# Performance work log

Measured on AMD Instinct MI355X. Metric: run time of the kernel, lower is better.

Reference implementation:

```python
import jax, jax.numpy as jnp
import numpy as np

L, M, K, H, F, D = 8, 32768, 8, 128, 32, 3  # fronts, nodes/front, in-degree, hidden, feat, depth-branches


def _resnet(x, w1, b1, w2, b2, w3, b3):
    # resnet module: lay3(tanh(lay2(tanh(lay1(x)))) + x)
    h1 = jnp.tanh(x @ w1 + b1)
    h2 = jnp.tanh(h1 @ w2 + b2)
    return (h2 + x) @ w3 + b3


def setup_inputs() -> dict:
    key = jax.random.key(0)
    ks = iter(jax.random.split(key, 80))

    def nrm(shape, fan_in):
        return jax.random.normal(next(ks), shape, jnp.float32) / np.float32(np.sqrt(fan_in))

    def bias(shape):
        return 0.01 * jax.random.normal(next(ks), shape, jnp.float32)

    inp = {}
    inp["node_feats"] = jax.random.normal(next(ks), (L, M, F), jnp.float32)
    inp["pred_idx"] = jax.random.randint(next(ks), (L - 1, M, K), 0, M, jnp.int32)
    inp["embed_w"] = nrm((F, H), F); inp["embed_b"] = bias((H,))
    # d{1,2,3}_mp_bwd and d{1,2,3}_mp_bwd1 : per-depth pair of H-resnets, stacked [D,2,...]
    inp["mp_w1"] = nrm((D, 2, H, H), H); inp["mp_b1"] = bias((D, 2, H))
    inp["mp_w2"] = nrm((D, 2, H, H), H); inp["mp_b2"] = bias((D, 2, H))
    inp["mp_w3"] = nrm((D, 2, H, H), H); inp["mp_b3"] = bias((D, 2, H))
    for p in ("comb", "node"):  # d*_comb_embed(+1), d*_node_embeds(+1)
        inp[p + "_wide_w1"] = nrm((D, 2 * H, 2 * H), 2 * H); inp[p + "_wide_b1"] = bias((D, 2 * H))
        inp[p + "_wide_w2"] = nrm((D, 2 * H, 2 * H), 2 * H); inp[p + "_wide_b2"] = bias((D, 2 * H))
        inp[p + "_wide_w3"] = nrm((D, 2 * H, H), 2 * H);     inp[p + "_wide_b3"] = bias((D, H))
        inp[p + "_h_w1"] = nrm((D, H, H), H); inp[p + "_h_b1"] = bias((D, H))
        inp[p + "_h_w2"] = nrm((D, H, H), H); inp[p + "_h_b2"] = bias((D, H))
        inp[p + "_h_w3"] = nrm((D, H, H), H); inp[p + "_h_b3"] = bias((D, H))
    return inp


def reference(node_feats, pred_idx, embed_w, embed_b,
              mp_w1, mp_b1, mp_w2, mp_b2, mp_w3, mp_b3,
              comb_wide_w1, comb_wide_b1, comb_wide_w2, comb_wide_b2, comb_wide_w3, comb_wide_b3,
              comb_h_w1, comb_h_b1, comb_h_w2, comb_h_b2, comb_h_w3, comb_h_b3,
              node_wide_w1, node_wide_b1, node_wide_w2, node_wide_b2, node_wide_w3, node_wide_b3,
              node_h_w1, node_h_b1, node_h_w2, node_h_b2, node_h_w3, node_h_b3):
    # front 0 (topological roots): apply_func only -> tanh(embed_op(feats))
    e = jnp.tanh(node_feats[0] @ embed_w + embed_b)          # [M, H]
    outs = [e]
    prev = e
    for l in range(1, L):
        d = min(l - 1, 2)                                    # bwd_depth branch (d1/d2/d3)
        # msg_func + redux_func: gather mailbox from predecessor front, sum-reduce, MLP
        s = prev[pred_idx[l - 1]].sum(axis=1)                # [M, K, H] -> [M, H]
        r = jnp.tanh(_resnet(s, mp_w1[d, 0], mp_b1[d, 0], mp_w2[d, 0], mp_b2[d, 0], mp_w3[d, 0], mp_b3[d, 0]))
        r = jnp.tanh(_resnet(r, mp_w1[d, 1], mp_b1[d, 1], mp_w2[d, 1], mp_b2[d, 1], mp_w3[d, 1], mp_b3[d, 1]))
        # apply_func: embed, comb branch (bwd_node_embeds is all-zero for not-yet-processed nodes),
        # then node_embeds branch on cat(embeds, msgs_redux)
        e = jnp.tanh(node_feats[l] @ embed_w + embed_b)
        c = jnp.concatenate([e, jnp.zeros_like(e)], axis=-1)  # [M, 2H]
        e = jnp.tanh(_resnet(c, comb_wide_w1[d], comb_wide_b1[d], comb_wide_w2[d], comb_wide_b2[d], comb_wide_w3[d], comb_wide_b3[d]))
        e = jnp.tanh(_resnet(e, comb_h_w1[d], comb_h_b1[d], comb_h_w2[d], comb_h_b2[d], comb_h_w3[d], comb_h_b3[d]))
        c2 = jnp.concatenate([e, r], axis=-1)                 # [M, 2H]
        e = jnp.tanh(_resnet(c2, node_wide_w1[d], node_wide_b1[d], node_wide_w2[d], node_wide_b2[d], node_wide_w3[d], node_wide_b3[d]))
        e = jnp.tanh(_resnet(e, node_h_w1[d], node_h_b1[d], node_h_w2[d], node_h_b2[d], node_h_w3[d], node_h_b3[d]))
        outs.append(e)
        prev = e
    return jnp.stack(outs)                                    # graph.ndata['bwd_node_embeds'] : [L, M, H]
```

## Files before the change

kernel.cpp:

```cpp
#include <hip/hip_runtime.h>
#include <hip/hip_bf16.h>

#define M_NODES 32768

using f16x8 = __attribute__((ext_vector_type(8))) _Float16;
using f16x4 = __attribute__((ext_vector_type(4))) _Float16;
using f32x4 = __attribute__((ext_vector_type(4))) float;
typedef unsigned short u16;
typedef unsigned int   u32;

__device__ __forceinline__ float h2f(u16 h){
  return (float)__builtin_bit_cast(_Float16, h);
}
__device__ __forceinline__ float tanh_fast(float x){
  float t = __builtin_amdgcn_exp2f(x * 2.8853900817779268f);
  return 1.0f - 2.0f * __builtin_amdgcn_rcpf(t + 1.0f);
}
__device__ __forceinline__ u16 f2h(float f){
  _Float16 h = (_Float16)f;
  return __builtin_bit_cast(u16, h);
}

struct PrepPtrs { const float* p[16]; };

__global__ void prep_kernel(PrepPtrs pp, u16* ws){
  const int Bc[16] = {1,6,6,6,3,3,3,3,3,3,3,3,3,3,3,3};
  const int Kc[16] = {32,128,128,128,256,256,256,128,128,128,256,256,256,128,128,128};
  const int Nc[16] = {128,128,128,128,256,256,128,128,128,128,256,256,128,128,128,128};
  const int tot = 1576960;
  for (int i = blockIdx.x*blockDim.x + threadIdx.x; i < tot; i += gridDim.x*blockDim.x){
    int e = i, s = 0;
    while (true){ int sz = Bc[s]*Kc[s]*Nc[s]; if (e < sz) break; e -= sz; ++s; }
    int K = Kc[s], N = Nc[s];
    int kn = K*N;
    int b = e / kn; int r2 = e - b*kn;
    int n = r2 / K; int k = r2 - n*K;
    float v = pp.p[s][(size_t)b*kn + (size_t)k*N + n];
    ws[i] = f2h(v);
  }
}

__global__ __launch_bounds__(256) void front0_kernel(const float* __restrict__ feats,
                                                     const float* __restrict__ ew,
                                                     const float* __restrict__ eb,
                                                     float* __restrict__ out){
  __shared__ float fl[2048];
  const int brow = blockIdx.x * 64;
  const float* f0 = feats + (size_t)brow*32;
#pragma unroll
  for (int it = 0; it < 2; ++it){
    int idx = threadIdx.x + it*256;
    *(float4*)(&fl[idx*4]) = *(const float4*)(f0 + idx*4);
  }
  __syncthreads();
  const int col = threadIdx.x & 127, rh = threadIdx.x >> 7;
  float w[32];
#pragma unroll
  for (int k = 0; k < 32; ++k) w[k] = ew[k*128 + col];
  const float bv = eb[col];
  for (int r = 0; r < 32; ++r){
    int row = rh*32 + r;
    float acc = bv;
#pragma unroll
    for (int k = 0; k < 32; ++k) acc += fl[row*32 + k] * w[k];
    out[(size_t)(brow + row)*128 + col] = tanh_fast(acc);
  }
}

struct WRing {
  const u16* wrow[4];
  f16x8 b0[4], b1[4];
};

template<int N, int WS, int NP>
__device__ __forceinline__ void wpreload(WRing& R, const u16* __restrict__ wt, int phase){
  const int tid  = threadIdx.x;
  const int lane = tid & 63, nq = tid >> 6;
  const int q = lane >> 4, c = lane & 15;
  constexpr int NT = N / 64;
  const int msk = NP - 1;
  const int p0 = phase & msk, p1 = (phase + 1) & msk;
#pragma unroll
  for (int j = 0; j < NT; ++j){
    int nt = nq*2 + (j & 1) + (j >> 1) * 8;
    R.wrow[j] = wt + (size_t)(nt*16 + c)*WS + q*8;
  }
#pragma unroll
  for (int j = 0; j < NT; ++j) R.b0[j] = *(const f16x8*)(R.wrow[j] + p0*32);
#pragma unroll
  for (int j = 0; j < NT; ++j) R.b1[j] = *(const f16x8*)(R.wrow[j] + p1*32);
}

template<int KLOOP, int N, int WS, int AMODE, int RESMODE, int OUTMODE, bool INPLACE,
         int NN, int NWS, int NNP>
__device__ __forceinline__ void mm_stage(const u16* inA, u16* outB, const u16* resB,
                                         const float* __restrict__ bias, float* gout,
                                         int phase, WRing& cur, WRing& nxt,
                                         const u16* __restrict__ wtnext)
{
  const int tid  = threadIdx.x;
  const int lane = tid & 63, nq = tid >> 6;
  const int q = lane >> 4, c = lane & 15;
  constexpr int NT = N / 64;
  constexpr int NP = KLOOP / 32;
  constexpr bool ABURST = (AMODE == 0 && NP == 4);
  const float* inAf = (const float*)inA;
  float*       outF = (float*)outB;
  const float* resF = (const float*)resB;
  const int msk = NP - 1;
  const int ph = phase & msk;

  f32x4 acc[4][NT];
#pragma unroll
  for (int m = 0; m < 4; ++m)
#pragma unroll
    for (int j = 0; j < NT; ++j) acc[m][j] = (f32x4){0.f,0.f,0.f,0.f};

  f16x8 aall[ABURST ? 16 : 1];
  if (ABURST){
#pragma unroll
    for (int kp = 0; kp < 4; ++kp){
      int kpp = (ph + kp) & 3;
#pragma unroll
      for (int m = 0; m < 4; ++m)
        aall[kp*4 + m] = *(const f16x8*)(&inA[(m*16 + c)*264 + kpp*32 + q*8]);
    }
  }

#pragma unroll
  for (int kp = 0; kp < NP; ++kp){
    const int kpp = (ph + kp) & msk;
    f16x8 bc[NT];
    if ((kp & 1) == 0){
#pragma unroll
      for (int j = 0; j < NT; ++j) bc[j] = cur.b0[j];
    } else {
#pragma unroll
      for (int j = 0; j < NT; ++j) bc[j] = cur.b1[j];
    }
    if (kp + 2 < NP){
      int kn = (ph + kp + 2) & msk;
      if ((kp & 1) == 0){
#pragma unroll
        for (int j = 0; j < NT; ++j) cur.b0[j] = *(const f16x8*)(cur.wrow[j] + kn*32);
      } else {
#pragma unroll
        for (int j = 0; j < NT; ++j) cur.b1[j] = *(const f16x8*)(cur.wrow[j] + kn*32);
      }
    }
#pragma unroll
    for (int m = 0; m < 4; ++m){
      if (AMODE == 0){
        f16x8 af;
        if (ABURST) af = aall[kp*4 + m];
        else        af = *(const f16x8*)(&inA[(m*16 + c)*264 + kpp*32 + q*8]);
#pragma unroll
        for (int j = 0; j < NT; ++j)
          acc[m][j] = __builtin_amdgcn_mfma_f32_16x16x32_f16(bc[j], af, acc[m][j], 0, 0, 0);
      } else {
        const float* ap = inAf + (m*16 + c)*132 + kpp*32 + q*8;
        float4 x0 = *(const float4*)(ap);
        float4 x1 = *(const float4*)(ap + 4);
        float xs[8] = {x0.x,x0.y,x0.z,x0.w,x1.x,x1.y,x1.z,x1.w};
        f16x8 ah, al;
#pragma unroll
        for (int k = 0; k < 8; ++k){
          _Float16 hi = (_Float16)xs[k];
          ah[k] = hi;
          al[k] = (_Float16)(xs[k] - (float)hi);
        }
#pragma unroll
        for (int j = 0; j < NT; ++j){
          acc[m][j] = __builtin_amdgcn_mfma_f32_16x16x32_f16(bc[j], ah, acc[m][j], 0, 0, 0);
          acc[m][j] = __builtin_amdgcn_mfma_f32_16x16x32_f16(bc[j], al, acc[m][j], 0, 0, 0);
        }
      }
    }
  }
  if constexpr (NN > 0) wpreload<NN, NWS, NNP>(nxt, wtnext, phase);
  if (INPLACE) __syncthreads();
#pragma unroll
  for (int j = 0; j < NT; ++j){
    int nt = nq*2 + (j & 1) + (j >> 1) * 8;
    int col0 = nt*16 + q*4;
    float4 bq = *(const float4*)(bias + col0);
    float bvv[4] = {bq.x, bq.y, bq.z, bq.w};
#pragma unroll
    for (int m = 0; m < 4; ++m){
      int row = m*16 + c;
      float v[4];
#pragma unroll
      for (int r = 0; r < 4; ++r) v[r] = tanh_fast(acc[m][j][r] + bvv[r]);
      if (RESMODE == 2 || (RESMODE == 1 && j < 2)){
        f16x4 rv = *(const f16x4*)(&resB[row*264 + col0]);
#pragma unroll
        for (int r = 0; r < 4; ++r) v[r] += (float)rv[r];
      } else if (RESMODE == 3){
        float4 rf = *(const float4*)(&resF[row*132 + col0]);
        v[0] += rf.x; v[1] += rf.y; v[2] += rf.z; v[3] += rf.w;
      }
      if (OUTMODE == 2){
        float4 o = {v[0], v[1], v[2], v[3]};
        *(float4*)(&gout[(size_t)row*128 + col0]) = o;
      } else if (OUTMODE == 1){
        float4 o = {v[0], v[1], v[2], v[3]};
        *(float4*)(&outF[row*132 + col0]) = o;
      } else {
        f16x4 h;
#pragma unroll
        for (int r = 0; r < 4; ++r) h[r] = (_Float16)v[r];
        *(f16x4*)(&outB[row*264 + col0]) = h;
      }
    }
  }
  __syncthreads();
}

__device__ __forceinline__ void embed_stage(const float* __restrict__ featsRow,
                                            u16* outB, const float* __restrict__ bias,
                                            int phase, WRing& cur, WRing& nxt,
                                            const u16* __restrict__ wtnext)
{
  const int tid  = threadIdx.x;
  const int lane = tid & 63, nq = tid >> 6;
  const int q = lane >> 4, c = lane & 15;
  f32x4 acc[4][2];
#pragma unroll
  for (int m = 0; m < 4; ++m){ acc[m][0] = (f32x4){0,0,0,0}; acc[m][1] = (f32x4){0,0,0,0}; }
#pragma unroll
  for (int m = 0; m < 4; ++m){
    int row = m*16 + c;
    const float* fp = featsRow + (size_t)row*32 + q*8;
    float4 a0 = *(const float4*)(fp);
    float4 a1 = *(const float4*)(fp + 4);
    float xs[8] = {a0.x,a0.y,a0.z,a0.w,a1.x,a1.y,a1.z,a1.w};
    f16x8 ah, al;
#pragma unroll
    for (int k = 0; k < 8; ++k){
      _Float16 hi = (_Float16)xs[k];
      ah[k] = hi;
      al[k] = (_Float16)(xs[k] - (float)hi);
    }
#pragma unroll
    for (int j = 0; j < 2; ++j){
      acc[m][j] = __builtin_amdgcn_mfma_f32_16x16x32_f16(cur.b0[j], ah, acc[m][j], 0, 0, 0);
      acc[m][j] = __builtin_amdgcn_mfma_f32_16x16x32_f16(cur.b0[j], al, acc[m][j], 0, 0, 0);
    }
  }
  wpreload<256, 256, 4>(nxt, wtnext, phase);
#pragma unroll
  for (int j = 0; j < 2; ++j){
    int nt = nq*2 + j;
    int col0 = nt*16 + q*4;
    float4 bq = *(const float4*)(bias + col0);
    float bvv[4] = {bq.x, bq.y, bq.z, bq.w};
#pragma unroll
    for (int m = 0; m < 4; ++m){
      int row = m*16 + c;
      f16x4 h;
#pragma unroll
      for (int r = 0; r < 4; ++r) h[r] = (_Float16)tanh_fast(acc[m][j][r] + bvv[r]);
      *(f16x4*)(&outB[row*264 + col0]) = h;
    }
  }
  __syncthreads();
}

struct FrontArgs {
  const float* feats; const int* pred;
  const u16* ws;
  float* out;
  const float* embed_b;
  const float* mp_b1; const float* mp_b2; const float* mp_b3;
  const float* cw_b1; const float* cw_b2; const float* cw_b3;
  const float* ch_b1; const float* ch_b2; const float* ch_b3;
  const float* nw_b1; const float* nw_b2; const float* nw_b3;
  const float* nh_b1; const float* nh_b2; const float* nh_b3;
  int l, d;
};

__global__ __launch_bounds__(256, 2) void front_kernel(FrontArgs A)
{
  extern __shared__ u16 lds[];
  u16* P  = lds;
  u16* Q  = lds + 16896;
  const int brow = blockIdx.x * 64;
  const int d = A.d;
  const u16* ws = A.ws;
  const int ph = blockIdx.x;
  const int d0 = d*2, d1 = d*2 + 1;

  WRing rA, rB;
  wpreload<128, 128, 4>(rA, ws + 4096 + (size_t)d0*16384, ph);

  {
    float* Pf = (float*)P;
    const float* prev = A.out + (size_t)(A.l - 1) * M_NODES * 128;
    const int c4 = threadIdx.x & 31;
    const int r0 = threadIdx.x >> 5;
#pragma unroll
    for (int rr = 0; rr < 8; ++rr){
      int row = r0 + rr*8;
      const int* ip = A.pred + ((size_t)(A.l - 1) * M_NODES + brow + row) * 8;
      float sx=0.f, sy=0.f, sz=0.f, sw=0.f;
#pragma unroll
      for (int p = 0; p < 8; ++p){
        const float4 v = *(const float4*)(prev + (size_t)ip[p]*128 + c4*4);
        sx += v.x; sy += v.y; sz += v.z; sw += v.w;
      }
      float4 o = {sx, sy, sz, sw};
      *(float4*)(&Pf[row*132 + c4*4]) = o;
    }
  }
  __syncthreads();

  mm_stage<128,128,128, 1,0,0,false, 128,128,4>(P, Q, nullptr, A.mp_b1 + d0*128, nullptr, ph, rA, rB, ws + 102400 + (size_t)d0*16384);
  mm_stage<128,128,128, 0,3,1,false, 128,128,4>(Q, P, P, A.mp_b2 + d0*128, nullptr, ph, rB, rA, ws + 200704 + (size_t)d0*16384);
  mm_stage<128,128,128, 1,0,0,false, 128,128,4>(P, Q, nullptr, A.mp_b3 + d0*128, nullptr, ph, rA, rB, ws + 4096 + (size_t)d1*16384);
  mm_stage<128,128,128, 0,0,0,false, 128,128,4>(Q, P, nullptr, A.mp_b1 + d1*128, nullptr, ph, rB, rA, ws + 102400 + (size_t)d1*16384);
  mm_stage<128,128,128, 0,2,1,true , 128,128,4>(P, P, Q, A.mp_b2 + d1*128, nullptr, ph, rA, rB, ws + 200704 + (size_t)d1*16384);
  mm_stage<128,128,128, 1,0,0,false, 128,32,1>(P, Q + 128, nullptr, A.mp_b3 + d1*128, nullptr, ph, rB, rA, ws);
  embed_stage(A.feats + ((size_t)A.l * M_NODES + brow) * 32, Q, A.embed_b, ph, rA, rB, ws + 299008 + (size_t)d*65536);
  mm_stage<128,256,256, 0,0,0,false, 256,256,8>(Q, P, nullptr, A.cw_b1 + d*256, nullptr, ph, rB, rA, ws + 495616 + (size_t)d*65536);
  mm_stage<256,256,256, 0,1,0,true , 128,256,8>(P, P, Q, A.cw_b2 + d*256, nullptr, ph, rA, rB, ws + 692224 + (size_t)d*32768);
  mm_stage<256,128,256, 0,0,0,false, 128,128,4>(P, Q, nullptr, A.cw_b3 + d*128, nullptr, ph, rB, rA, ws + 790528 + (size_t)d*16384);
  mm_stage<128,128,128, 0,0,0,false, 128,128,4>(Q, P, nullptr, A.ch_b1 + d*128, nullptr, ph, rA, rB, ws + 839680 + (size_t)d*16384);
  mm_stage<128,128,128, 0,2,0,true , 128,128,4>(P, P, Q, A.ch_b2 + d*128, nullptr, ph, rB, rA, ws + 888832 + (size_t)d*16384);
  mm_stage<128,128,128, 0,0,0,false, 256,256,8>(P, Q, nullptr, A.ch_b3 + d*128, nullptr, ph, rA, rB, ws + 937984 + (size_t)d*65536);
  mm_stage<256,256,256, 0,0,0,false, 256,256,8>(Q, P, nullptr, A.nw_b1 + d*256, nullptr, ph, rB, rA, ws + 1134592 + (size_t)d*65536);
  mm_stage<256,256,256, 0,2,0,true , 128,256,8>(P, P, Q, A.nw_b2 + d*256, nullptr, ph, rA, rB, ws + 1331200 + (size_t)d*32768);
  mm_stage<256,128,256, 0,0,0,false, 128,128,4>(P, Q, nullptr, A.nw_b3 + d*128, nullptr, ph, rB, rA, ws + 1429504 + (size_t)d*16384);
  mm_stage<128,128,128, 0,0,0,false, 128,128,4>(Q, P, nullptr, A.nh_b1 + d*128, nullptr, ph, rA, rB, ws + 1478656 + (size_t)d*16384);
  mm_stage<128,128,128, 0,2,0,true , 128,128,4>(P, P, Q, A.nh_b2 + d*128, nullptr, ph, rB, rA, ws + 1527808 + (size_t)d*16384);
  float* gout = A.out + ((size_t)A.l * M_NODES + brow) * 128;
  mm_stage<128,128,128, 0,0,2,false, 0,0,1>(P, nullptr, nullptr, A.nh_b3 + d*128, gout, ph, rA, rB, nullptr);
}

extern "C" void kernel_launch(void* const* d_in, const int* in_sizes, int n_in,
                              void* d_out, int out_size, void* d_ws, size_t ws_size,
                              hipStream_t stream)
{
  (void)in_sizes; (void)n_in; (void)out_size; (void)ws_size;
  const float* feats = (const float*)d_in[0];
  const int*   pred  = (const int*)d_in[1];
  u16*   ws  = (u16*)d_ws;
  float* out = (float*)d_out;

  PrepPtrs pp;
  const int wIdx[16] = {2,4,6,8,10,12,14,16,18,20,22,24,26,28,30,32};
  for (int i = 0; i < 16; ++i) pp.p[i] = (const float*)d_in[wIdx[i]];
  prep_kernel<<<2048, 256, 0, stream>>>(pp, ws);

  front0_kernel<<<M_NODES/64, 256, 0, stream>>>(feats, (const float*)d_in[2], (const float*)d_in[3], out);

  const size_t LDSB = (size_t)(2*64*264) * sizeof(u16);
  (void)hipFuncSetAttribute((const void*)front_kernel,
                            hipFuncAttributeMaxDynamicSharedMemorySize, (int)LDSB);

  FrontArgs A;
  A.feats = feats; A.pred = pred; A.ws = ws; A.out = out;
  A.embed_b = (const float*)d_in[3];
  A.mp_b1 = (const float*)d_in[5];  A.mp_b2 = (const float*)d_in[7];  A.mp_b3 = (const float*)d_in[9];
  A.cw_b1 = (const float*)d_in[11]; A.cw_b2 = (const float*)d_in[13]; A.cw_b3 = (const float*)d_in[15];
  A.ch_b1 = (const float*)d_in[17]; A.ch_b2 = (const float*)d_in[19]; A.ch_b3 = (const float*)d_in[21];
  A.nw_b1 = (const float*)d_in[23]; A.nw_b2 = (const float*)d_in[25]; A.nw_b3 = (const float*)d_in[27];
  A.nh_b1 = (const float*)d_in[29]; A.nh_b2 = (const float*)d_in[31]; A.nh_b3 = (const float*)d_in[33];

  for (int l = 1; l < 8; ++l){
    A.l = l;
    A.d = (l - 1 < 2) ? (l - 1) : 2;
    front_kernel<<<M_NODES/64, 256, LDSB, stream>>>(A);
  }
}
```

Baseline: 645.1 us.

## Preload full next-stage weight fragments into registers and use lighter LDS barriers

Replaces the two-slot rotating weight ring, which had a per-block phase offset and refilled itself inside the K loop, with per-stage register fragments. Each stage's weights are loaded in full during the previous stage's epilogue. The largest 256x256 stages keep a ring variant to limit register pressure. __syncthreads is replaced by a barrier that waits only on LDS counters, so global loads in flight are not drained at each stage boundary. Dropping the phase staggering may raise L2 contention, and the larger register footprint may lower occupancy.

```diff
diff --git a/kernel.cpp b/kernel.cpp
--- a/kernel.cpp
+++ b/kernel.cpp
@@ -9,6 +9,10 @@
 typedef unsigned short u16;
 typedef unsigned int   u32;
 
+__device__ __forceinline__ u16 f2h(float f){
+  _Float16 h = (_Float16)f;
+  return __builtin_bit_cast(u16, h);
+}
 __device__ __forceinline__ float h2f(u16 h){
   return (float)__builtin_bit_cast(_Float16, h);
 }
@@ -16,9 +20,12 @@
   float t = __builtin_amdgcn_exp2f(x * 2.8853900817779268f);
   return 1.0f - 2.0f * __builtin_amdgcn_rcpf(t + 1.0f);
 }
-__device__ __forceinline__ u16 f2h(float f){
-  _Float16 h = (_Float16)f;
-  return __builtin_bit_cast(u16, h);
+
+__device__ __forceinline__ void barL(){
+  asm volatile("" ::: "memory");
+  asm volatile("s_waitcnt lgkmcnt(0)");
+  __builtin_amdgcn_s_barrier();
+  asm volatile("" ::: "memory");
 }
 
 struct PrepPtrs { const float* p[16]; };
@@ -67,36 +74,42 @@
   }
 }
 
-struct WRing {
-  const u16* wrow[4];
-  f16x8 b0[4], b1[4];
-};
-
-template<int N, int WS, int NP>
-__device__ __forceinline__ void wpreload(WRing& R, const u16* __restrict__ wt, int phase){
-  const int tid  = threadIdx.x;
-  const int lane = tid & 63, nq = tid >> 6;
+template<int NPAN, int NT> struct WF { const u16* wrow[NT]; f16x8 b[NPAN][NT]; };
+
+template<int NPAN, int NT, int WS>
+__device__ __forceinline__ void wload(WF<NPAN,NT>& R, const u16* __restrict__ wt){
+  const int tid = threadIdx.x, lane = tid & 63, nq = tid >> 6;
   const int q = lane >> 4, c = lane & 15;
-  constexpr int NT = N / 64;
-  const int msk = NP - 1;
-  const int p0 = phase & msk, p1 = (phase + 1) & msk;
 #pragma unroll
   for (int j = 0; j < NT; ++j){
     int nt = nq*2 + (j & 1) + (j >> 1) * 8;
     R.wrow[j] = wt + (size_t)(nt*16 + c)*WS + q*8;
   }
 #pragma unroll
-  for (int j = 0; j < NT; ++j) R.b0[j] = *(const f16x8*)(R.wrow[j] + p0*32);
-#pragma unroll
-  for (int j = 0; j < NT; ++j) R.b1[j] = *(const f16x8*)(R.wrow[j] + p1*32);
-}
-
-template<int KLOOP, int N, int WS, int AMODE, int RESMODE, int OUTMODE, bool INPLACE,
-         int NN, int NWS, int NNP>
-__device__ __forceinline__ void mm_stage(const u16* inA, u16* outB, const u16* resB,
-                                         const float* __restrict__ bias, float* gout,
-                                         int phase, WRing& cur, WRing& nxt,
-                                         const u16* __restrict__ wtnext)
+  for (int p = 0; p < NPAN; ++p)
+#pragma unroll
+    for (int j = 0; j < NT; ++j) R.b[p][j] = *(const f16x8*)(R.wrow[j] + p*32);
+}
+
+struct WR4 { const u16* wrow[4]; f16x8 b0[4], b1[4]; };
+__device__ __forceinline__ void wring_init(WR4& R, const u16* __restrict__ wt){
+  const int tid = threadIdx.x, lane = tid & 63, nq = tid >> 6;
+  const int q = lane >> 4, c = lane & 15;
+#pragma unroll
+  for (int j = 0; j < 4; ++j){
+    int nt = nq*2 + (j & 1) + (j >> 1) * 8;
+    R.wrow[j] = wt + (size_t)(nt*16 + c)*256 + q*8;
+  }
+#pragma unroll
+  for (int j = 0; j < 4; ++j) R.b0[j] = *(const f16x8*)(R.wrow[j]);
+#pragma unroll
+  for (int j = 0; j < 4; ++j) R.b1[j] = *(const f16x8*)(R.wrow[j] + 32);
+}
+
+template<int KLOOP, int N, int WS, int AMODE, int RESMODE, int OUTMODE, bool INPLACE, typename F>
+__device__ __forceinline__ void stageF(const u16* inA, u16* outB, const u16* resB,
+                                       const float* __restrict__ bias, float* gout,
+                                       WF<KLOOP/32, N/64>& W, F&& pre)
 {
   const int tid  = threadIdx.x;
   const int lane = tid & 63, nq = tid >> 6;
@@ -107,8 +120,6 @@
   const float* inAf = (const float*)inA;
   float*       outF = (float*)outB;
   const float* resF = (const float*)resB;
-  const int msk = NP - 1;
-  const int ph = phase & msk;
 
   f32x4 acc[4][NT];
 #pragma unroll
@@ -119,46 +130,25 @@
   f16x8 aall[ABURST ? 16 : 1];
   if (ABURST){
 #pragma unroll
-    for (int kp = 0; kp < 4; ++kp){
-      int kpp = (ph + kp) & 3;
+    for (int kp = 0; kp < 4; ++kp)
 #pragma unroll
       for (int m = 0; m < 4; ++m)
-        aall[kp*4 + m] = *(const f16x8*)(&inA[(m*16 + c)*264 + kpp*32 + q*8]);
-    }
+        aall[kp*4 + m] = *(const f16x8*)(&inA[(m*16 + c)*264 + kp*32 + q*8]);
   }
 
 #pragma unroll
   for (int kp = 0; kp < NP; ++kp){
-    const int kpp = (ph + kp) & msk;
-    f16x8 bc[NT];
-    if ((kp & 1) == 0){
-#pragma unroll
-      for (int j = 0; j < NT; ++j) bc[j] = cur.b0[j];
-    } else {
-#pragma unroll
-      for (int j = 0; j < NT; ++j) bc[j] = cur.b1[j];
-    }
-    if (kp + 2 < NP){
-      int kn = (ph + kp + 2) & msk;
-      if ((kp & 1) == 0){
-#pragma unroll
-        for (int j = 0; j < NT; ++j) cur.b0[j] = *(const f16x8*)(cur.wrow[j] + kn*32);
-      } else {
-#pragma unroll
-        for (int j = 0; j < NT; ++j) cur.b1[j] = *(const f16x8*)(cur.wrow[j] + kn*32);
-      }
-    }
 #pragma unroll
     for (int m = 0; m < 4; ++m){
       if (AMODE == 0){
         f16x8 af;
         if (ABURST) af = aall[kp*4 + m];
-        else        af = *(const f16x8*)(&inA[(m*16 + c)*264 + kpp*32 + q*8]);
+        else        af = *(const f16x8*)(&inA[(m*16 + c)*264 + kp*32 + q*8]);
 #pragma unroll
         for (int j = 0; j < NT; ++j)
-          acc[m][j] = __builtin_amdgcn_mfma_f32_16x16x32_f16(bc[j], af, acc[m][j], 0, 0, 0);
+          acc[m][j] = __builtin_amdgcn_mfma_f32_16x16x32_f16(W.b[kp][j], af, acc[m][j], 0, 0, 0);
       } else {
-        const float* ap = inAf + (m*16 + c)*132 + kpp*32 + q*8;
+        const float* ap = inAf + (m*16 + c)*132 + kp*32 + q*8;
         float4 x0 = *(const float4*)(ap);
         float4 x1 = *(const float4*)(ap + 4);
         float xs[8] = {x0.x,x0.y,x0.z,x0.w,x1.x,x1.y,x1.z,x1.w};
@@ -171,14 +161,14 @@
         }
 #pragma unroll
         for (int j = 0; j < NT; ++j){
-          acc[m][j] = __builtin_amdgcn_mfma_f32_16x16x32_f16(bc[j], ah, acc[m][j], 0, 0, 0);
-          acc[m][j] = __builtin_amdgcn_mfma_f32_16x16x32_f16(bc[j], al, acc[m][j], 0, 0, 0);
+          acc[m][j] = __builtin_amdgcn_mfma_f32_16x16x32_f16(W.b[kp][j], ah, acc[m][j], 0, 0, 0);
+          acc[m][j] = __builtin_amdgcn_mfma_f32_16x16x32_f16(W.b[kp][j], al, acc[m][j], 0, 0, 0);
         }
       }
     }
   }
-  if constexpr (NN > 0) wpreload<NN, NWS, NNP>(nxt, wtnext, phase);
-  if (INPLACE) __syncthreads();
+  pre();
+  if (INPLACE) barL();
 #pragma unroll
   for (int j = 0; j < NT; ++j){
     int nt = nq*2 + (j & 1) + (j >> 1) * 8;
@@ -213,13 +203,82 @@
       }
     }
   }
-  __syncthreads();
-}
-
+  barL();
+}
+
+template<int RESMODE, bool INPLACE, typename F>
+__device__ __forceinline__ void stageR(const u16* inA, u16* outB, const u16* resB,
+                                       const float* __restrict__ bias, WR4& W, F&& pre)
+{
+  const int tid  = threadIdx.x;
+  const int lane = tid & 63, nq = tid >> 6;
+  const int q = lane >> 4, c = lane & 15;
+
+  f32x4 acc[4][4];
+#pragma unroll
+  for (int m = 0; m < 4; ++m)
+#pragma unroll
+    for (int j = 0; j < 4; ++j) acc[m][j] = (f32x4){0.f,0.f,0.f,0.f};
+
+#pragma unroll
+  for (int kp = 0; kp < 8; ++kp){
+    f16x8 bc[4];
+    if ((kp & 1) == 0){
+#pragma unroll
+      for (int j = 0; j < 4; ++j) bc[j] = W.b0[j];
+    } else {
+#pragma unroll
+      for (int j = 0; j < 4; ++j) bc[j] = W.b1[j];
+    }
+    if (kp + 2 < 8){
+      if ((kp & 1) == 0){
+#pragma unroll
+        for (int j = 0; j < 4; ++j) W.b0[j] = *(const f16x8*)(W.wrow[j] + (kp + 2)*32);
+      } else {
+#pragma unroll
+        for (int j = 0; j < 4; ++j) W.b1[j] = *(const f16x8*)(W.wrow[j] + (kp + 2)*32);
+      }
+    }
+#pragma unroll
+    for (int m = 0; m < 4; ++m){
+      f16x8 af = *(const f16x8*)(&inA[(m*16 + c)*264 + kp*32 + q*8]);
+#pragma unroll
+      for (int j = 0; j < 4; ++j)
+        acc[m][j] = __builtin_amdgcn_mfma_f32_16x16x32_f16(bc[j], af, acc[m][j], 0, 0, 0);
+    }
+  }
+  pre();
+  if (INPLACE) barL();
+#pragma unroll
+  for (int j = 0; j < 4; ++j){
+    int nt = nq*2 + (j & 1) + (j >> 1) * 8;
+    int col0 = nt*16 + q*4;
+    float4 bq = *(const float4*)(bias + col0);
+    float bvv[4] = {bq.x, bq.y, bq.z, bq.w};
+#pragma unroll
+    for (int m = 0; m < 4; ++m){
+      int row = m*16 + c;
+      float v[4];
+#pragma unroll
+      for (int r = 0; r < 4; ++r) v[r] = tanh_fast(acc[m][j][r] + bvv[r]);
+      if (RESMODE == 2 || (RESMODE == 1 && j < 2)){
+        f16x4 rv = *(const f16x4*)(&resB[row*264 + col0]);
+#pragma unroll
+        for (int r = 0; r < 4; ++r) v[r] += (float)rv[r];
+      }
+      f16x4 h;
+#pragma unroll
+      for (int r = 0; r < 4; ++r) h[r] = (_Float16)v[r];
+      *(f16x4*)(&outB[row*264 + col0]) = h;
+    }
+  }
+  barL();
+}
+
+template<typename F>
 __device__ __forceinline__ void embed_stage(const float* __restrict__ featsRow,
                                             u16* outB, const float* __restrict__ bias,
-                                            int phase, WRing& cur, WRing& nxt,
-                                            const u16* __restrict__ wtnext)
+                                            WF<1,2>& W, F&& pre)
 {
   const int tid  = threadIdx.x;
   const int lane = tid & 63, nq = tid >> 6;
@@ -243,11 +302,11 @@
     }
 #pragma unroll
     for (int j = 0; j < 2; ++j){
-      acc[m][j] = __builtin_amdgcn_mfma_f32_16x16x32_f16(cur.b0[j], ah, acc[m][j], 0, 0, 0);
-      acc[m][j] = __builtin_amdgcn_mfma_f32_16x16x32_f16(cur.b0[j], al, acc[m][j], 0, 0, 0);
-    }
-  }
-  wpreload<256, 256, 4>(nxt, wtnext, phase);
+      acc[m][j] = __builtin_amdgcn_mfma_f32_16x16x32_f16(W.b[0][j], ah, acc[m][j], 0, 0, 0);
+      acc[m][j] = __builtin_amdgcn_mfma_f32_16x16x32_f16(W.b[0][j], al, acc[m][j], 0, 0, 0);
+    }
+  }
+  pre();
 #pragma unroll
   for (int j = 0; j < 2; ++j){
     int nt = nq*2 + j;
@@ -263,7 +322,7 @@
       *(f16x4*)(&outB[row*264 + col0]) = h;
     }
   }
-  __syncthreads();
+  barL();
 }
 
 struct FrontArgs {
@@ -287,11 +346,15 @@
   const int brow = blockIdx.x * 64;
   const int d = A.d;
   const u16* ws = A.ws;
-  const int ph = blockIdx.x;
   const int d0 = d*2, d1 = d*2 + 1;
 
-  WRing rA, rB;
-  wpreload<128, 128, 4>(rA, ws + 4096 + (size_t)d0*16384, ph);
+  WF<4,2> w1, w2, w3, w4, w5, w6, wch1, wch2, wch3, wnh1, wnh2, wnh3;
+  WF<1,2> wemb;
+  WF<4,4> wcw1;
+  WF<8,2> wcw3, wnw3;
+  WR4 rcw2, rnw1, rnw2;
+
+  wload<4,2,128>(w1, ws + 4096 + (size_t)d0*16384);
 
   {
     float* Pf = (float*)P;
@@ -312,28 +375,46 @@
       *(float4*)(&Pf[row*132 + c4*4]) = o;
     }
   }
-  __syncthreads();
-
-  mm_stage<128,128,128, 1,0,0,false, 128,128,4>(P, Q, nullptr, A.mp_b1 + d0*128, nullptr, ph, rA, rB, ws + 102400 + (size_t)d0*16384);
-  mm_stage<128,128,128, 0,3,1,false, 128,128,4>(Q, P, P, A.mp_b2 + d0*128, nullptr, ph, rB, rA, ws + 200704 + (size_t)d0*16384);
-  mm_stage<128,128,128, 1,0,0,false, 128,128,4>(P, Q, nullptr, A.mp_b3 + d0*128, nullptr, ph, rA, rB, ws + 4096 + (size_t)d1*16384);
-  mm_stage<128,128,128, 0,0,0,false, 128,128,4>(Q, P, nullptr, A.mp_b1 + d1*128, nullptr, ph, rB, rA, ws + 102400 + (size_t)d1*16384);
-  mm_stage<128,128,128, 0,2,1,true , 128,128,4>(P, P, Q, A.mp_b2 + d1*128, nullptr, ph, rA, rB, ws + 200704 + (size_t)d1*16384);
-  mm_stage<128,128,128, 1,0,0,false, 128,32,1>(P, Q + 128, nullptr, A.mp_b3 + d1*128, nullptr, ph, rB, rA, ws);
-  embed_stage(A.feats + ((size_t)A.l * M_NODES + brow) * 32, Q, A.embed_b, ph, rA, rB, ws + 299008 + (size_t)d*65536);
-  mm_stage<128,256,256, 0,0,0,false, 256,256,8>(Q, P, nullptr, A.cw_b1 + d*256, nullptr, ph, rB, rA, ws + 495616 + (size_t)d*65536);
-  mm_stage<256,256,256, 0,1,0,true , 128,256,8>(P, P, Q, A.cw_b2 + d*256, nullptr, ph, rA, rB, ws + 692224 + (size_t)d*32768);
-  mm_stage<256,128,256, 0,0,0,false, 128,128,4>(P, Q, nullptr, A.cw_b3 + d*128, nullptr, ph, rB, rA, ws + 790528 + (size_t)d*16384);
-  mm_stage<128,128,128, 0,0,0,false, 128,128,4>(Q, P, nullptr, A.ch_b1 + d*128, nullptr, ph, rA, rB, ws + 839680 + (size_t)d*16384);
-  mm_stage<128,128,128, 0,2,0,true , 128,128,4>(P, P, Q, A.ch_b2 + d*128, nullptr, ph, rB, rA, ws + 888832 + (size_t)d*16384);
-  mm_stage<128,128,128, 0,0,0,false, 256,256,8>(P, Q, nullptr, A.ch_b3 + d*128, nullptr, ph, rA, rB, ws + 937984 + (size_t)d*65536);
-  mm_stage<256,256,256, 0,0,0,false, 256,256,8>(Q, P, nullptr, A.nw_b1 + d*256, nullptr, ph, rB, rA, ws + 1134592 + (size_t)d*65536);
-  mm_stage<256,256,256, 0,2,0,true , 128,256,8>(P, P, Q, A.nw_b2 + d*256, nullptr, ph, rA, rB, ws + 1331200 + (size_t)d*32768);
-  mm_stage<256,128,256, 0,0,0,false, 128,128,4>(P, Q, nullptr, A.nw_b3 + d*128, nullptr, ph, rB, rA, ws + 1429504 + (size_t)d*16384);
-  mm_stage<128,128,128, 0,0,0,false, 128,128,4>(Q, P, nullptr, A.nh_b1 + d*128, nullptr, ph, rA, rB, ws + 1478656 + (size_t)d*16384);
-  mm_stage<128,128,128, 0,2,0,true , 128,128,4>(P, P, Q, A.nh_b2 + d*128, nullptr, ph, rB, rA, ws + 1527808 + (size_t)d*16384);
+  barL();
+
+  stageF<128,128,128, 1,0,0,false>(P, Q, nullptr, A.mp_b1 + d0*128, nullptr, w1,
+    [&]{ wload<4,2,128>(w2, ws + 102400 + (size_t)d0*16384); });
+  stageF<128,128,128, 0,3,1,false>(Q, P, P, A.mp_b2 + d0*128, nullptr, w2,
+    [&]{ wload<4,2,128>(w3, ws + 200704 + (size_t)d0*16384); });
+  stageF<128,128,128, 1,0,0,false>(P, Q, nullptr, A.mp_b3 + d0*128, nullptr, w3,
+    [&]{ wload<4,2,128>(w4, ws + 4096 + (size_t)d1*16384); });
+  stageF<128,128,128, 0,0,0,false>(Q, P, nullptr, A.mp_b1 + d1*128, nullptr, w4,
+    [&]{ wload<4,2,128>(w5, ws + 102400 + (size_t)d1*16384); });
+  stageF<128,128,128, 0,2,1,true >(P, P, Q, A.mp_b2 + d1*128, nullptr, w5,
+    [&]{ wload<4,2,128>(w6, ws + 200704 + (size_t)d1*16384); });
+  stageF<128,128,128, 1,0,0,false>(P, Q + 128, nullptr, A.mp_b3 + d1*128, nullptr, w6,
+    [&]{ wload<1,2,32>(wemb, ws); });
+  embed_stage(A.feats + ((size_t)A.l * M_NODES + brow) * 32, Q, A.embed_b, wemb,
+    [&]{ wload<4,4,256>(wcw1, ws + 299008 + (size_t)d*65536); });
+  stageF<128,256,256, 0,0,0,false>(Q, P, nullptr, A.cw_b1 + d*256, nullptr, wcw1,
+    [&]{ wring_init(rcw2, ws + 495616 + (size_t)d*65536); });
+  stageR<1,true>(P, P, Q, A.cw_b2 + d*256, rcw2,
+    [&]{ wload<8,2,256>(wcw3, ws + 692224 + (size_t)d*32768); });
+  stageF<256,128,256, 0,0,0,false>(P, Q, nullptr, A.cw_b3 + d*128, nullptr, wcw3,
+    [&]{ wload<4,2,128>(wch1, ws + 790528 + (size_t)d*16384); });
+  stageF<128,128,128, 0,0,0,false>(Q, P, nullptr, A.ch_b1 + d*128, nullptr, wch1,
+    [&]{ wload<4,2,128>(wch2, ws + 839680 + (size_t)d*16384); });
+  stageF<128,128,128, 0,2,0,true >(P, P, Q, A.ch_b2 + d*128, nullptr, wch2,
+    [&]{ wload<4,2,128>(wch3, ws + 888832 + (size_t)d*16384); });
+  stageF<128,128,128, 0,0,0,false>(P, Q, nullptr, A.ch_b3 + d*128, nullptr, wch3,
+    [&]{ wring_init(rnw1, ws + 937984 + (size_t)d*65536); });
+  stageR<0,false>(Q, P, nullptr, A.nw_b1 + d*256, rnw1,
+    [&]{ wring_init(rnw2, ws + 1134592 + (size_t)d*65536); });
+  stageR<2,true>(P, P, Q, A.nw_b2 + d*256, rnw2,
+    [&]{ wload<8,2,256>(wnw3, ws + 1331200 + (size_t)d*32768); });
+  stageF<256,128,256, 0,0,0,false>(P, Q, nullptr, A.nw_b3 + d*128, nullptr, wnw3,
+    [&]{ wload<4,2,128>(wnh1, ws + 1429504 + (size_t)d*16384); });
+  stageF<128,128,128, 0,0,0,false>(Q, P, nullptr, A.nh_b1 + d*128, nullptr, wnh1,
+    [&]{ wload<4,2,128>(wnh2, ws + 1478656 + (size_t)d*16384); });
+  stageF<128,128,128, 0,2,0,true >(P, P, Q, A.nh_b2 + d*128, nullptr, wnh2,
+    [&]{ wload<4,2,128>(wnh3, ws + 1527808 + (size_t)d*16384); });
   float* gout = A.out + ((size_t)A.l * M_NODES + brow) * 128;
-  mm_stage<128,128,128, 0,0,2,false, 0,0,1>(P, nullptr, nullptr, A.nh_b3 + d*128, gout, ph, rA, rB, nullptr);
+  stageF<128,128,128, 0,0,2,false>(P, nullptr, nullptr, A.nh_b3 + d*128, gout, wnh3, []{});
 }
 
 extern "C" void kernel_launch(void* const* d_in, const int* in_sizes, int n_in,
```

Measured after the change: 660.4 us. +2.4%, slower.
